# Optimization experiments

Hardware: AMD Instinct MI355X
Metric: run time of the kernel (lower is better)

The kernel has to match this reference:

```python
import jax, jax.numpy as jnp
import numpy as np

HEADS = 8
EPS = 1e-5
PW1 = (512, 8, 14, 14)   # (C, T, H, W), C = headsize1 * heads
PW2 = (512, 32, 7, 7)


def _ln(x, g, b):
    m = jnp.mean(x, axis=-1, keepdims=True)
    v = jnp.var(x, axis=-1, keepdims=True)
    return (x - m) * jax.lax.rsqrt(v + EPS) * g + b


def _mha(q, k, v):
    b, nq, c = q.shape
    nk = k.shape[1]
    hd = c // HEADS
    qh = q.reshape(b, nq, HEADS, hd).transpose(0, 2, 1, 3)  # [b,h,nq,hd]
    kh = k.reshape(b, nk, HEADS, hd).transpose(0, 2, 1, 3)
    vh = v.reshape(b, nk, HEADS, hd).transpose(0, 2, 1, 3)
    s = jnp.einsum('bhqd,bhkd->bhqk', qh, kh) * (hd ** -0.5)
    a = jax.nn.softmax(s, axis=-1)
    o = jnp.einsum('bhqk,bhkd->bhqd', a, vh)
    return o.transpose(0, 2, 1, 3).reshape(b, nq, c)


def _tok(x):
    b, c, t, h, w = x.shape
    return x.transpose(0, 2, 3, 4, 1).reshape(b, t * h * w, c)


def _detok(t, c, T, H, W):
    b = t.shape[0]
    return t.reshape(b, T, H, W, c).transpose(0, 4, 1, 2, 3)


def _out_head(y, w, bias, bn_g, bn_b):
    # 1x1x1 Conv3d + ReLU + BatchNorm3d (eval, running mean 0 / var 1)
    z = jnp.einsum('bcthw,oc->bothw', y, w) + bias[None, :, None, None, None]
    z = jax.nn.relu(z)
    z = z * jax.lax.rsqrt(jnp.float32(1.0 + EPS))
    return z * bn_g[None, :, None, None, None] + bn_b[None, :, None, None, None]


def reference(x1, x2, Wq1, bq1, Wk1, bk1, Wv1, bv1, ln1_g, ln1_b,
              Wq2, bq2, Wk2, bk2, Wv2, bv2, ln2_g, ln2_b,
              out1_w, out1_b, bn1_g, bn1_b, out2_w, out2_b, bn2_g, bn2_b):
    t1 = _tok(x1)  # [B, 1568, 512]
    t2 = _tok(x2)  # [B, 1568, 512]
    for i in range(3):  # three chained norm + cross-attn stages
        q1 = _ln(t1, ln1_g[i], ln1_b[i]) @ Wq1[i].T + bq1[i]
        k1 = t2 @ Wk1[i].T + bk1[i]
        v1 = t2 @ Wv1[i].T + bv1[i]
        q2 = _ln(t2, ln2_g[i], ln2_b[i]) @ Wq2[i].T + bq2[i]
        k2 = t1 @ Wk2[i].T + bk2[i]
        v2 = t1 @ Wv2[i].T + bv2[i]
        t1 = t1 + _mha(q1, k1, v1)
        t2 = t2 + _mha(q2, k2, v2)
    y1 = _detok(t1, *PW1)
    y2 = _detok(t2, *PW2)
    z1 = _out_head(y1, out1_w, out1_b, bn1_g, bn1_b)
    z2 = _out_head(y2, out2_w, out2_b, bn2_g, bn2_b)
    return (z1, z2)


def setup_inputs() -> dict:
    key = jax.random.key(0)
    ks = jax.random.split(key, 12)
    C = 512
    w = lambda k, shp: jax.random.normal(k, shp, jnp.float32) * 0.02
    return {
        'x1': jax.random.normal(ks[0], (4, C, 8, 14, 14), jnp.float32),
        'x2': jax.random.normal(ks[1], (4, C, 32, 7, 7), jnp.float32),
        'Wq1': w(ks[2], (3, C, C)), 'bq1': jnp.zeros((3, C), jnp.float32),
        'Wk1': w(ks[3], (3, C, C)), 'bk1': jnp.zeros((3, C), jnp.float32),
        'Wv1': w(ks[4], (3, C, C)), 'bv1': jnp.zeros((3, C), jnp.float32),
        'ln1_g': jnp.ones((3, C), jnp.float32), 'ln1_b': jnp.zeros((3, C), jnp.float32),
        'Wq2': w(ks[5], (3, C, C)), 'bq2': jnp.zeros((3, C), jnp.float32),
        'Wk2': w(ks[6], (3, C, C)), 'bk2': jnp.zeros((3, C), jnp.float32),
        'Wv2': w(ks[7], (3, C, C)), 'bv2': jnp.zeros((3, C), jnp.float32),
        'ln2_g': jnp.ones((3, C), jnp.float32), 'ln2_b': jnp.zeros((3, C), jnp.float32),
        'out1_w': w(ks[8], (C, C)), 'out1_b': jnp.zeros((C,), jnp.float32),
        'bn1_g': jnp.ones((C,), jnp.float32), 'bn1_b': jnp.zeros((C,), jnp.float32),
        'out2_w': w(ks[9], (C, C)), 'out2_b': jnp.zeros((C,), jnp.float32),
        'bn2_g': jnp.ones((C,), jnp.float32), 'bn2_b': jnp.zeros((C,), jnp.float32),
    }
```

## Files before the change

### kernel.cpp

```cpp
#include <hip/hip_runtime.h>

typedef __bf16 bf16_t;
typedef __bf16 bf16x8 __attribute__((ext_vector_type(8)));
typedef __bf16 bf16x4 __attribute__((ext_vector_type(4)));
typedef float f32x4 __attribute__((ext_vector_type(4)));
typedef float f32x16 __attribute__((ext_vector_type(16)));
typedef unsigned u32x4 __attribute__((ext_vector_type(4)));

#define NTOK 1568
#define CDIM 512
#define BATCH 4
#define MROWS (BATCH*NTOK)
#define RSQ1PEPS 0.9999950000374997f
#define CEXP 0.1803368801111204f
#define DEFER_THR 44.3614195558365f

__device__ __forceinline__ float fexp2(float x) {
  float r;
  asm("v_exp_f32 %0, %1" : "=v"(r) : "v"(x));
  return r;
}

__device__ __forceinline__ void glds16(const bf16_t* src, bf16_t* dst) {
  __builtin_amdgcn_global_load_lds(
      (const __attribute__((address_space(1))) unsigned*)src,
      (__attribute__((address_space(3))) unsigned*)dst, 16, 0, 0);
}

struct CastArgs { const float* s[20]; };
__global__ __launch_bounds__(256) void cast_kernel(CastArgs ca, bf16_t* __restrict__ out) {
  int idx = blockIdx.x * 256 + threadIdx.x;
  int m = idx >> 16;
  const float4* sp = (const float4*)ca.s[m];
  float4 v = sp[idx & 65535];
  bf16x4 o;
  o[0] = (bf16_t)v.x; o[1] = (bf16_t)v.y; o[2] = (bf16_t)v.z; o[3] = (bf16_t)v.w;
  *(bf16x4*)(out + (size_t)idx * 4) = o;
}

struct TokArgs { const float* x[2]; float* tf[2]; bf16_t* tb[2]; };
__global__ __launch_bounds__(256) void tok_kernel(TokArgs ta) {
  __shared__ float tile[32][33];
  int z = blockIdx.z, sel = z >> 2, b = z & 3;
  int c0 = blockIdx.y * 32, s0 = blockIdx.x * 32;
  int tx = threadIdx.x, ty = threadIdx.y;
  const float* xp = ta.x[sel] + (size_t)b * CDIM * NTOK;
  for (int r = 0; r < 32; r += 8)
    tile[ty + r][tx] = xp[(size_t)(c0 + ty + r) * NTOK + s0 + tx];
  __syncthreads();
  float* tfp = ta.tf[sel] + (size_t)b * NTOK * CDIM;
  bf16_t* tbp = ta.tb[sel] + (size_t)b * NTOK * CDIM;
  for (int r = 0; r < 32; r += 8) {
    float v = tile[tx][ty + r];
    size_t idx = (size_t)(s0 + ty + r) * CDIM + c0 + tx;
    tfp[idx] = v;
    tbp[idx] = (bf16_t)v;
  }
}

__global__ __launch_bounds__(64) void ln_kernel(
    const float* __restrict__ t1, const float* __restrict__ t2,
    const float* __restrict__ g1, const float* __restrict__ b1,
    const float* __restrict__ g2, const float* __restrict__ b2,
    bf16_t* __restrict__ o1, bf16_t* __restrict__ o2) {
  int row = blockIdx.x;
  const float* t; const float* g; const float* bt; bf16_t* out;
  if (row < MROWS) { t = t1; g = g1; bt = b1; out = o1; }
  else { row -= MROWS; t = t2; g = g2; bt = b2; out = o2; }
  int l = threadIdx.x;
  const float* x = t + (size_t)row * CDIM;
  float4 v0 = ((const float4*)x)[l];
  float4 v1 = ((const float4*)x)[l + 64];
  float s = v0.x + v0.y + v0.z + v0.w + v1.x + v1.y + v1.z + v1.w;
  float sq = v0.x*v0.x + v0.y*v0.y + v0.z*v0.z + v0.w*v0.w
           + v1.x*v1.x + v1.y*v1.y + v1.z*v1.z + v1.w*v1.w;
  for (int m = 1; m < 64; m <<= 1) { s += __shfl_xor(s, m); sq += __shfl_xor(sq, m); }
  float mean = s * (1.f / 512.f);
  float var = sq * (1.f / 512.f) - mean * mean;
  float rs = rsqrtf(var + 1e-5f);
  float4 g0 = ((const float4*)g)[l], g1v = ((const float4*)g)[l + 64];
  float4 b0 = ((const float4*)bt)[l], b1v = ((const float4*)bt)[l + 64];
  bf16x4 o0, o1v;
  o0[0] = (bf16_t)((v0.x - mean) * rs * g0.x + b0.x);
  o0[1] = (bf16_t)((v0.y - mean) * rs * g0.y + b0.y);
  o0[2] = (bf16_t)((v0.z - mean) * rs * g0.z + b0.z);
  o0[3] = (bf16_t)((v0.w - mean) * rs * g0.w + b0.w);
  o1v[0] = (bf16_t)((v1.x - mean) * rs * g1v.x + b1v.x);
  o1v[1] = (bf16_t)((v1.y - mean) * rs * g1v.y + b1v.y);
  o1v[2] = (bf16_t)((v1.z - mean) * rs * g1v.z + b1v.z);
  o1v[3] = (bf16_t)((v1.w - mean) * rs * g1v.w + b1v.w);
  *(bf16x4*)(out + (size_t)row * CDIM + l * 4) = o0;
  *(bf16x4*)(out + (size_t)row * CDIM + 256 + l * 4) = o1v;
}

template<int MODE>
__device__ __forceinline__ void gemm_core(
    bf16_t (* __restrict__ As)[40], bf16_t (* __restrict__ Bs)[40],
    const bf16_t* __restrict__ A, const bf16_t* __restrict__ Bp,
    const float* __restrict__ bias, const float* __restrict__ bng,
    const float* __restrict__ bnb, bf16_t* __restrict__ outb,
    float* __restrict__ outf, int m0, int n0, int Nvalid) {
  int tid = threadIdx.x;
  int w = tid >> 6, l = tid & 63, lr = l & 15, kg = l >> 4;
  int wm = (w >> 1) * 64, wn = (w & 1) * 64;
  f32x4 acc[4][4];
  for (int i = 0; i < 4; i++)
    for (int j = 0; j < 4; j++)
      acc[i][j] = f32x4{0.f, 0.f, 0.f, 0.f};
  int srow = tid >> 1;
  int soff = (tid & 1) * 16;
  int brow = n0 + srow;
  if (MODE != 0 && brow >= Nvalid) brow = Nvalid - 1;
  const bf16_t* aq = A + (size_t)(m0 + srow) * CDIM + soff;
  const bf16_t* bq = Bp + (size_t)brow * CDIM + soff;
  for (int kk = 0; kk < 16; kk++) {
    __syncthreads();
    bf16x8 a0 = *(const bf16x8*)(aq);
    bf16x8 a1 = *(const bf16x8*)(aq + 8);
    bf16x8 b0 = *(const bf16x8*)(bq);
    bf16x8 b1 = *(const bf16x8*)(bq + 8);
    aq += 32; bq += 32;
    *(bf16x8*)&As[srow][soff] = a0;
    *(bf16x8*)&As[srow][soff + 8] = a1;
    *(bf16x8*)&Bs[srow][soff] = b0;
    *(bf16x8*)&Bs[srow][soff + 8] = b1;
    __syncthreads();
    bf16x8 af[4], bfr[4];
    for (int i = 0; i < 4; i++) af[i] = *(const bf16x8*)&As[wm + i * 16 + lr][kg * 8];
    for (int j = 0; j < 4; j++) bfr[j] = *(const bf16x8*)&Bs[wn + j * 16 + lr][kg * 8];
    for (int i = 0; i < 4; i++)
      for (int j = 0; j < 4; j++)
        acc[i][j] = __builtin_amdgcn_mfma_f32_16x16x32_bf16(af[i], bfr[j], acc[i][j], 0, 0, 0);
  }
  for (int i = 0; i < 4; i++)
    for (int j = 0; j < 4; j++) {
      int rbase = m0 + wm + i * 16 + kg * 4;
      int col = n0 + wn + j * 16 + lr;
      for (int r = 0; r < 4; r++) {
        int row = rbase + r;
        float v = acc[i][j][r];
        if (MODE == 0) {
          v += bias[col];
          outb[(size_t)row * CDIM + col] = (bf16_t)v;
        } else if (MODE == 1) {
          v += bias[row];
          v = v > 0.f ? v : 0.f;
          v *= RSQ1PEPS;
          v = v * bng[row] + bnb[row];
          if (col < Nvalid) outf[(size_t)row * NTOK + col] = v;
        } else {
          v += bias[row];
          if (col < Nvalid) outb[(size_t)row * NTOK + col] = (bf16_t)v;
        }
      }
    }
}

struct ProjArgs {
  const bf16_t* A0[4]; const bf16_t* W0[4]; const float* b0[4]; bf16_t* o0[4];
  const bf16_t* W2[2]; const bf16_t* B2[2]; const float* b2[2]; bf16_t* o2[2];
};
__global__ __launch_bounds__(256) void proj_kernel(ProjArgs p) {
  __shared__ bf16_t As[128][40];
  __shared__ bf16_t Bs[128][40];
  int id = blockIdx.x;
  if (id < 784) {
    int set = id / 196, rem = id % 196;
    int n0 = (rem & 3) * 128, m0 = (rem >> 2) * 128;
    gemm_core<0>(As, Bs, p.A0[set], p.W0[set], p.b0[set], nullptr, nullptr,
                 p.o0[set], nullptr, m0, n0, 512);
  } else {
    int j = id - 784;
    int unit = j / 52;
    int which = unit >> 2, bat = unit & 3;
    int rem = j % 52;
    int n0 = (rem % 13) * 128, m0 = (rem / 13) * 128;
    gemm_core<2>(As, Bs, p.W2[which], p.B2[which] + (size_t)bat * NTOK * CDIM,
                 p.b2[which], nullptr, nullptr,
                 p.o2[which] + (size_t)bat * CDIM * NTOK, nullptr, m0, n0, NTOK);
  }
}

__global__ __launch_bounds__(256) void head_kernel(
    const bf16_t* __restrict__ W1, const bf16_t* __restrict__ W2,
    const bf16_t* __restrict__ t1b, const bf16_t* __restrict__ t2b,
    const float* __restrict__ b1, const float* __restrict__ b2,
    const float* __restrict__ bng1, const float* __restrict__ bnb1,
    const float* __restrict__ bng2, const float* __restrict__ bnb2,
    float* __restrict__ out) {
  __shared__ bf16_t As[128][40];
  __shared__ bf16_t Bs[128][40];
  int z = blockIdx.z;
  int which = z >> 2, bat = z & 3;
  const bf16_t* A = which ? W2 : W1;
  const bf16_t* Bp = (which ? t2b : t1b) + (size_t)bat * NTOK * CDIM;
  const float* bias = which ? b2 : b1;
  const float* bng = which ? bng2 : bng1;
  const float* bnb = which ? bnb2 : bnb1;
  float* outf = out + (size_t)which * BATCH * CDIM * NTOK + (size_t)bat * CDIM * NTOK;
  int m0 = blockIdx.y * 128, n0 = blockIdx.x * 128;
  gemm_core<1>(As, Bs, A, Bp, bias, bng, bnb, nullptr, outf, m0, n0, NTOK);
}

__device__ __forceinline__ float tree_max16(const f32x16& s) {
  float a0 = fmaxf(s[0], s[1]), a1 = fmaxf(s[2], s[3]);
  float a2 = fmaxf(s[4], s[5]), a3 = fmaxf(s[6], s[7]);
  float a4 = fmaxf(s[8], s[9]), a5 = fmaxf(s[10], s[11]);
  float a6 = fmaxf(s[12], s[13]), a7 = fmaxf(s[14], s[15]);
  a0 = fmaxf(a0, a1); a2 = fmaxf(a2, a3); a4 = fmaxf(a4, a5); a6 = fmaxf(a6, a7);
  return fmaxf(fmaxf(a0, a2), fmaxf(a4, a6));
}

__device__ __forceinline__ void build_frags(const float* p, bf16x8& Fa, bf16x8& Fb) {
  unsigned pk[8];
#pragma unroll
  for (int g = 0; g < 8; g++) {
    union { bf16_t hh[2]; unsigned u; } cv;
    cv.hh[0] = (bf16_t)p[2 * g];
    cv.hh[1] = (bf16_t)p[2 * g + 1];
    pk[g] = cv.u;
  }
  asm volatile("v_permlane32_swap_b32 %0, %1" : "+v"(pk[0]), "+v"(pk[2]));
  asm volatile("v_permlane32_swap_b32 %0, %1" : "+v"(pk[1]), "+v"(pk[3]));
  asm volatile("v_permlane32_swap_b32 %0, %1" : "+v"(pk[4]), "+v"(pk[6]));
  asm volatile("v_permlane32_swap_b32 %0, %1" : "+v"(pk[5]), "+v"(pk[7]));
  union { u32x4 u; bf16x8 bv; } A, B;
  A.u[0] = pk[0]; A.u[1] = pk[1]; A.u[2] = pk[2]; A.u[3] = pk[3];
  B.u[0] = pk[4]; B.u[1] = pk[5]; B.u[2] = pk[6]; B.u[3] = pk[7];
  Fa = A.bv; Fb = B.bv;
}

struct AttnArgs {
  const bf16_t* q[2]; const bf16_t* k[2]; const bf16_t* v[2];
  float* tf[2]; bf16_t* tb[2];
};

#define STAGE(TN, SL)                                                         \
  {                                                                           \
    int tnS_ = (TN); if (tnS_ > 48) tnS_ = 48;                                \
    glds16(kgl + (size_t)tnS_ * (32 * CDIM), &Ks[SL][wq8][0]);                \
    glds16(vgl + tnS_ * 32, &Vs[SL][wq16][0]);                                \
  }

#define QK(SL, SA)                                                            \
  {                                                                           \
    const bf16_t* kr_ = &Ks[SL][lo][0];                                       \
    __builtin_amdgcn_s_setprio(1);                                            \
    SA = __builtin_amdgcn_mfma_f32_32x32x16_bf16(                             \
        *(const bf16x8*)(kr_ + ((hi * 8) ^ sw3)), qf[0], z, 0, 0, 0);         \
    SA = __builtin_amdgcn_mfma_f32_32x32x16_bf16(                             \
        *(const bf16x8*)(kr_ + ((16 + hi * 8) ^ sw3)), qf[1], SA, 0, 0, 0);   \
    SA = __builtin_amdgcn_mfma_f32_32x32x16_bf16(                             \
        *(const bf16x8*)(kr_ + ((32 + hi * 8) ^ sw3)), qf[2], SA, 0, 0, 0);   \
    SA = __builtin_amdgcn_mfma_f32_32x32x16_bf16(                             \
        *(const bf16x8*)(kr_ + ((48 + hi * 8) ^ sw3)), qf[3], SA, 0, 0, 0);   \
    __builtin_amdgcn_s_setprio(0);                                            \
  }

#define FIN(SA, SL)                                                           \
  {                                                                           \
    float tm_ = tree_max16(SA);                                               \
    tm_ = fmaxf(tm_, __shfl_xor(tm_, 32));                                    \
    if (!__all(tm_ <= m_i + DEFER_THR)) {                                     \
      float mn_ = fmaxf(m_i, tm_);                                            \
      float al_ = fexp2((m_i - mn_) * CEXP);                                  \
      _Pragma("unroll")                                                       \
      for (int r_ = 0; r_ < 16; r_++) { ot0[r_] *= al_; ot1[r_] *= al_; }     \
      l_i *= al_;                                                             \
      m_i = mn_;                                                              \
    }                                                                         \
    float nmC_ = -m_i * CEXP;                                                 \
    float pa_[16];                                                            \
    _Pragma("unroll")                                                         \
    for (int r_ = 0; r_ < 16; r_++) pa_[r_] = fexp2(fmaf(SA[r_], CEXP, nmC_));\
    float ts_ = ((pa_[0]+pa_[1])+(pa_[2]+pa_[3]))+((pa_[4]+pa_[5])+(pa_[6]+pa_[7]))\
              + ((pa_[8]+pa_[9])+(pa_[10]+pa_[11]))+((pa_[12]+pa_[13])+(pa_[14]+pa_[15]));\
    ts_ += __shfl_xor(ts_, 32);                                               \
    l_i += ts_;                                                               \
    bf16x8 F0_, F1_;                                                          \
    build_frags(pa_, F0_, F1_);                                               \
    __builtin_amdgcn_s_setprio(1);                                            \
    ot0 = __builtin_amdgcn_mfma_f32_32x32x16_bf16(                            \
        *(const bf16x8*)(&Vs[SL][lo][(hi * 8) ^ sw2]), F0_, ot0, 0, 0, 0);    \
    ot0 = __builtin_amdgcn_mfma_f32_32x32x16_bf16(                            \
        *(const bf16x8*)(&Vs[SL][lo][(16 + hi * 8) ^ sw2]), F1_, ot0, 0, 0, 0);\
    ot1 = __builtin_amdgcn_mfma_f32_32x32x16_bf16(                            \
        *(const bf16x8*)(&Vs[SL][32 + lo][(hi * 8) ^ sw2]), F0_, ot1, 0, 0, 0);\
    ot1 = __builtin_amdgcn_mfma_f32_32x32x16_bf16(                            \
        *(const bf16x8*)(&Vs[SL][32 + lo][(16 + hi * 8) ^ sw2]), F1_, ot1, 0, 0, 0);\
    __builtin_amdgcn_s_setprio(0);                                            \
  }

#define STEP(T, SACUR, SAPRV, QSL, FSL, SSL)                                  \
  {                                                                           \
    STAGE((T) + 2, SSL);                                                      \
    QK(QSL, SACUR);                                                           \
    FIN(SAPRV, FSL);                                                          \
    asm volatile("s_waitcnt vmcnt(2)" ::: "memory");                          \
    __builtin_amdgcn_s_barrier();                                             \
  }

__global__ __launch_bounds__(256) void attn_kernel(AttnArgs aa) {
  __shared__ alignas(16) bf16_t Ks[4][32][64];
  __shared__ alignas(16) bf16_t Vs[4][64][32];
  int id = blockIdx.x;
  int xcd = id & 7, sl = id >> 3;
  int g = xcd + ((sl / 13) << 3);
  int qt = sl % 13;
  int ss = g >> 5, b = (g >> 3) & 3, h = g & 7;
  const bf16_t* qg = aa.q[ss];
  const bf16_t* kgp = aa.k[ss];
  const bf16_t* vtg = aa.v[ss];
  float* tf = aa.tf[ss];
  bf16_t* tb = aa.tb[ss];
  int tid = threadIdx.x, w = tid >> 6, l = tid & 63;
  int lo = l & 31, hi = l >> 5;
  int wq8 = w * 8, wq16 = w * 16;
  int sw3 = (lo & 7) << 3, sw2 = (lo & 3) << 3;
  const size_t kbase = ((size_t)b * NTOK) * CDIM + h * 64;
  const size_t vbase = ((size_t)b * CDIM + h * 64) * NTOK;

  int q0 = qt * 128 + w * 32;
  int qrow = q0 + lo;
  int qr = qrow < NTOK ? qrow : NTOK - 1;
  const bf16_t* qp = qg + kbase + (size_t)qr * CDIM + hi * 8;
  bf16x8 qf[4];
  qf[0] = *(const bf16x8*)(qp);
  qf[1] = *(const bf16x8*)(qp + 16);
  qf[2] = *(const bf16x8*)(qp + 32);
  qf[3] = *(const bf16x8*)(qp + 48);
  asm volatile("" : "+v"(qf[0]), "+v"(qf[1]), "+v"(qf[2]), "+v"(qf[3]));
  asm volatile("s_waitcnt vmcnt(0)" ::: "memory");

  const bf16_t* kgl = kgp + kbase + (size_t)(wq8 + (l >> 3)) * CDIM
                      + (((l & 7) ^ ((l >> 3) & 7)) << 3);
  const bf16_t* vgl = vtg + vbase + (size_t)(wq16 + (l >> 2)) * NTOK
                      + (((l & 3) ^ ((l >> 2) & 3)) << 3);

  float m_i = -3.0e38f, l_i = 0.f;
  f32x16 ot0, ot1, z, saA, saB;
#pragma unroll
  for (int r = 0; r < 16; r++) { ot0[r] = 0.f; ot1[r] = 0.f; z[r] = 0.f; }

  STAGE(0, 0);
  STAGE(1, 1);
  STAGE(2, 2);
  asm volatile("s_waitcnt vmcnt(2)" ::: "memory");
  __builtin_amdgcn_s_barrier();
  QK(0, saA);

  for (int t = 1; t <= 45; t += 4) {
    STEP(t + 0, saB, saA, 1, 0, 3);
    STEP(t + 1, saA, saB, 2, 1, 0);
    STEP(t + 2, saB, saA, 3, 2, 1);
    STEP(t + 3, saA, saB, 0, 3, 2);
  }
  FIN(saA, 0);

  if (qrow < NTOK) {
    float inv = 1.f / l_i;
    float* tfp = tf + ((size_t)b * NTOK + qrow) * CDIM + h * 64 + hi * 4;
    bf16_t* tbp = tb + ((size_t)b * NTOK + qrow) * CDIM + h * 64 + hi * 4;
#pragma unroll
    for (int db = 0; db < 2; db++) {
#pragma unroll
      for (int gq = 0; gq < 4; gq++) {
        int doff = db * 32 + gq * 8;
        float4 old = *(float4*)(tfp + doff);
        float4 nv;
        float a0 = (db ? ot1[gq * 4 + 0] : ot0[gq * 4 + 0]) * inv;
        float a1 = (db ? ot1[gq * 4 + 1] : ot0[gq * 4 + 1]) * inv;
        float a2 = (db ? ot1[gq * 4 + 2] : ot0[gq * 4 + 2]) * inv;
        float a3 = (db ? ot1[gq * 4 + 3] : ot0[gq * 4 + 3]) * inv;
        nv.x = old.x + a0; nv.y = old.y + a1; nv.z = old.z + a2; nv.w = old.w + a3;
        *(float4*)(tfp + doff) = nv;
        bf16x4 ob;
        ob[0] = (bf16_t)nv.x; ob[1] = (bf16_t)nv.y;
        ob[2] = (bf16_t)nv.z; ob[3] = (bf16_t)nv.w;
        *(bf16x4*)(tbp + doff) = ob;
      }
    }
  }
}

extern "C" void kernel_launch(void* const* d_in, const int* in_sizes, int n_in,
                              void* d_out, int out_size, void* d_ws, size_t ws_size,
                              hipStream_t stream) {
  (void)in_sizes; (void)n_in; (void)out_size; (void)ws_size;
  const float* x1 = (const float*)d_in[0];
  const float* x2 = (const float*)d_in[1];
  const float* Wq1 = (const float*)d_in[2];
  const float* bq1 = (const float*)d_in[3];
  const float* Wk1 = (const float*)d_in[4];
  const float* bk1 = (const float*)d_in[5];
  const float* Wv1 = (const float*)d_in[6];
  const float* bv1 = (const float*)d_in[7];
  const float* ln1_g = (const float*)d_in[8];
  const float* ln1_b = (const float*)d_in[9];
  const float* Wq2 = (const float*)d_in[10];
  const float* bq2 = (const float*)d_in[11];
  const float* Wk2 = (const float*)d_in[12];
  const float* bk2 = (const float*)d_in[13];
  const float* Wv2 = (const float*)d_in[14];
  const float* bv2 = (const float*)d_in[15];
  const float* ln2_g = (const float*)d_in[16];
  const float* ln2_b = (const float*)d_in[17];
  const float* out1_w = (const float*)d_in[18];
  const float* out1_b = (const float*)d_in[19];
  const float* bn1_g = (const float*)d_in[20];
  const float* bn1_b = (const float*)d_in[21];
  const float* out2_w = (const float*)d_in[22];
  const float* out2_b = (const float*)d_in[23];
  const float* bn2_g = (const float*)d_in[24];
  const float* bn2_b = (const float*)d_in[25];

  const size_t WMAT = 512 * 512;
  char* ws = (char*)d_ws;
  bf16_t* wb = (bf16_t*)ws;
  size_t off = 20 * WMAT * sizeof(bf16_t);
  float* t1f = (float*)(ws + off); off += (size_t)MROWS * CDIM * 4;
  float* t2f = (float*)(ws + off); off += (size_t)MROWS * CDIM * 4;
  bf16_t* t1b = (bf16_t*)(ws + off); off += (size_t)MROWS * CDIM * 2;
  bf16_t* t2b = (bf16_t*)(ws + off); off += (size_t)MROWS * CDIM * 2;
  bf16_t* l1b = (bf16_t*)(ws + off); off += (size_t)MROWS * CDIM * 2;
  bf16_t* l2b = (bf16_t*)(ws + off); off += (size_t)MROWS * CDIM * 2;
  bf16_t* q1b = (bf16_t*)(ws + off); off += (size_t)MROWS * CDIM * 2;
  bf16_t* k1b = (bf16_t*)(ws + off); off += (size_t)MROWS * CDIM * 2;
  bf16_t* v1b = (bf16_t*)(ws + off); off += (size_t)MROWS * CDIM * 2;
  bf16_t* q2b = (bf16_t*)(ws + off); off += (size_t)MROWS * CDIM * 2;
  bf16_t* k2b = (bf16_t*)(ws + off); off += (size_t)MROWS * CDIM * 2;
  bf16_t* v2b = (bf16_t*)(ws + off); off += (size_t)MROWS * CDIM * 2;

  CastArgs ca;
  for (int i = 0; i < 3; i++) {
    ca.s[0 + i] = Wq1 + (size_t)i * WMAT;
    ca.s[3 + i] = Wk1 + (size_t)i * WMAT;
    ca.s[6 + i] = Wv1 + (size_t)i * WMAT;
    ca.s[9 + i] = Wq2 + (size_t)i * WMAT;
    ca.s[12 + i] = Wk2 + (size_t)i * WMAT;
    ca.s[15 + i] = Wv2 + (size_t)i * WMAT;
  }
  ca.s[18] = out1_w;
  ca.s[19] = out2_w;
  cast_kernel<<<5120, 256, 0, stream>>>(ca, wb);

  TokArgs ta;
  ta.x[0] = x1; ta.x[1] = x2;
  ta.tf[0] = t1f; ta.tf[1] = t2f;
  ta.tb[0] = t1b; ta.tb[1] = t2b;
  tok_kernel<<<dim3(49, 16, 8), dim3(32, 8), 0, stream>>>(ta);

  AttnArgs aa;
  aa.q[0] = q1b; aa.q[1] = q2b;
  aa.k[0] = k1b; aa.k[1] = k2b;
  aa.v[0] = v1b; aa.v[1] = v2b;
  aa.tf[0] = t1f; aa.tf[1] = t2f;
  aa.tb[0] = t1b; aa.tb[1] = t2b;

  for (int i = 0; i < 3; i++) {
    ln_kernel<<<2 * MROWS, 64, 0, stream>>>(t1f, t2f,
        ln1_g + i * 512, ln1_b + i * 512, ln2_g + i * 512, ln2_b + i * 512,
        l1b, l2b);
    ProjArgs pa;
    pa.A0[0] = l1b; pa.W0[0] = wb + (0 + i) * WMAT; pa.b0[0] = bq1 + i * 512; pa.o0[0] = q1b;
    pa.A0[1] = t2b; pa.W0[1] = wb + (3 + i) * WMAT; pa.b0[1] = bk1 + i * 512; pa.o0[1] = k1b;
    pa.A0[2] = l2b; pa.W0[2] = wb + (9 + i) * WMAT; pa.b0[2] = bq2 + i * 512; pa.o0[2] = q2b;
    pa.A0[3] = t1b; pa.W0[3] = wb + (12 + i) * WMAT; pa.b0[3] = bk2 + i * 512; pa.o0[3] = k2b;
    pa.W2[0] = wb + (6 + i) * WMAT; pa.B2[0] = t2b; pa.b2[0] = bv1 + i * 512; pa.o2[0] = v1b;
    pa.W2[1] = wb + (15 + i) * WMAT; pa.B2[1] = t1b; pa.b2[1] = bv2 + i * 512; pa.o2[1] = v2b;
    proj_kernel<<<1200, 256, 0, stream>>>(pa);
    attn_kernel<<<832, 256, 0, stream>>>(aa);
  }

  float* out = (float*)d_out;
  head_kernel<<<dim3(13, 4, 8), 256, 0, stream>>>(
      wb + 18 * WMAT, wb + 19 * WMAT, t1b, t2b,
      out1_b, out2_b, bn1_g, bn1_b, bn2_g, bn2_b, out);
}
```

Baseline: 452.5 us.

## Split attention KV range in two and merge with LayerNorm-fused combine kernel

The attention kernel now splits each query tile's 49 key tiles into two halves processed by separate blocks (1664 instead of 832). It writes unnormalized bf16 partial outputs plus per-row max and sum to workspace. A new combine kernel merges the two partials with log-sum-exp weights, adds the residual, writes the fp32 and bf16 token copies, and computes the next stage's LayerNorm, which replaces the separate ln_kernel launch inside the loop. The aim is more parallelism on the 256-CU part and one fewer full pass over the tokens. The cost is a partial-output round trip through memory, an extra launch per stage, and bf16 rounding of the unnormalized partial outputs.

Measured after the change: 467.1 us. 3.2% more time.

```diff
diff --git a/kernel.cpp b/kernel.cpp
--- a/kernel.cpp
+++ b/kernel.cpp
@@ -14,6 +14,7 @@
 #define RSQ1PEPS 0.9999950000374997f
 #define CEXP 0.1803368801111204f
 #define DEFER_THR 44.3614195558365f
+#define PROWS 200704
 
 __device__ __forceinline__ float fexp2(float x) {
   float r;
@@ -232,14 +233,12 @@
 
 struct AttnArgs {
   const bf16_t* q[2]; const bf16_t* k[2]; const bf16_t* v[2];
-  float* tf[2]; bf16_t* tb[2];
 };
 
 #define STAGE(TN, SL)                                                         \
   {                                                                           \
-    int tnS_ = (TN); if (tnS_ > 48) tnS_ = 48;                                \
-    glds16(kgl + (size_t)tnS_ * (32 * CDIM), &Ks[SL][wq8][0]);                \
-    glds16(vgl + tnS_ * 32, &Vs[SL][wq16][0]);                                \
+    glds16(kgl + (size_t)(TN) * (32 * CDIM), &Ks[SL][wq8][0]);                \
+    glds16(vgl + (TN) * 32, &Vs[SL][wq16][0]);                                \
   }
 
 #define QK(SL, SA)                                                            \
@@ -291,28 +290,46 @@
     __builtin_amdgcn_s_setprio(0);                                            \
   }
 
-#define STEP(T, SACUR, SAPRV, QSL, FSL, SSL)                                  \
-  {                                                                           \
-    STAGE((T) + 2, SSL);                                                      \
-    QK(QSL, SACUR);                                                           \
-    FIN(SAPRV, FSL);                                                          \
-    asm volatile("s_waitcnt vmcnt(2)" ::: "memory");                          \
-    __builtin_amdgcn_s_barrier();                                             \
-  }
-
-__global__ __launch_bounds__(256) void attn_kernel(AttnArgs aa) {
+template<int NT>
+__device__ __forceinline__ void attn_core(
+    const bf16_t* kgl, const bf16_t* vgl,
+    bf16_t (*Ks)[32][64], bf16_t (*Vs)[64][32],
+    const bf16x8* qf, int lo, int hi, int sw3, int sw2, int wq8, int wq16,
+    float& m_i, float& l_i, f32x16& ot0, f32x16& ot1, const f32x16& z) {
+  f32x16 saA, saB;
+  STAGE(0, 0);
+  STAGE(1, 1);
+  STAGE(2, 2);
+  asm volatile("s_waitcnt vmcnt(2)" ::: "memory");
+  __builtin_amdgcn_s_barrier();
+  QK(0, saA);
+#pragma unroll
+  for (int t = 1; t < NT; ++t) {
+    int tn = (t + 2 > NT - 1) ? (NT - 1) : (t + 2);
+    STAGE(tn, (t + 2) & 3);
+    if (t & 1) { QK(t & 3, saB); FIN(saA, (t - 1) & 3); }
+    else       { QK(t & 3, saA); FIN(saB, (t - 1) & 3); }
+    asm volatile("s_waitcnt vmcnt(2)" ::: "memory");
+    __builtin_amdgcn_s_barrier();
+  }
+  if ((NT - 1) & 1) { FIN(saB, (NT - 1) & 3); }
+  else              { FIN(saA, (NT - 1) & 3); }
+}
+
+__global__ __launch_bounds__(256) void attn_kernel(
+    AttnArgs aa, bf16_t* __restrict__ po, float* __restrict__ pm,
+    float* __restrict__ pl) {
   __shared__ alignas(16) bf16_t Ks[4][32][64];
   __shared__ alignas(16) bf16_t Vs[4][64][32];
   int id = blockIdx.x;
   int xcd = id & 7, sl = id >> 3;
-  int g = xcd + ((sl / 13) << 3);
-  int qt = sl % 13;
+  int g = xcd + ((sl / 26) << 3);
+  int rem = sl % 26;
+  int qt = rem >> 1, sp = rem & 1;
   int ss = g >> 5, b = (g >> 3) & 3, h = g & 7;
   const bf16_t* qg = aa.q[ss];
   const bf16_t* kgp = aa.k[ss];
   const bf16_t* vtg = aa.v[ss];
-  float* tf = aa.tf[ss];
-  bf16_t* tb = aa.tb[ss];
   int tid = threadIdx.x, w = tid >> 6, l = tid & 63;
   int lo = l & 31, hi = l >> 5;
   int wq8 = w * 8, wq16 = w * 16;
@@ -338,48 +355,108 @@
                       + (((l & 3) ^ ((l >> 2) & 3)) << 3);
 
   float m_i = -3.0e38f, l_i = 0.f;
-  f32x16 ot0, ot1, z, saA, saB;
+  f32x16 ot0, ot1, z;
 #pragma unroll
   for (int r = 0; r < 16; r++) { ot0[r] = 0.f; ot1[r] = 0.f; z[r] = 0.f; }
 
-  STAGE(0, 0);
-  STAGE(1, 1);
-  STAGE(2, 2);
-  asm volatile("s_waitcnt vmcnt(2)" ::: "memory");
-  __builtin_amdgcn_s_barrier();
-  QK(0, saA);
-
-  for (int t = 1; t <= 45; t += 4) {
-    STEP(t + 0, saB, saA, 1, 0, 3);
-    STEP(t + 1, saA, saB, 2, 1, 0);
-    STEP(t + 2, saB, saA, 3, 2, 1);
-    STEP(t + 3, saA, saB, 0, 3, 2);
-  }
-  FIN(saA, 0);
+  if (sp == 0) {
+    attn_core<25>(kgl, vgl, Ks, Vs, qf, lo, hi, sw3, sw2, wq8, wq16,
+                  m_i, l_i, ot0, ot1, z);
+  } else {
+    attn_core<24>(kgl + (size_t)25 * 32 * CDIM, vgl + 25 * 32, Ks, Vs,
+                  qf, lo, hi, sw3, sw2, wq8, wq16,
+                  m_i, l_i, ot0, ot1, z);
+  }
 
   if (qrow < NTOK) {
-    float inv = 1.f / l_i;
-    float* tfp = tf + ((size_t)b * NTOK + qrow) * CDIM + h * 64 + hi * 4;
-    bf16_t* tbp = tb + ((size_t)b * NTOK + qrow) * CDIM + h * 64 + hi * 4;
+    size_t prow = ((((size_t)ss * 4 + b) * 8 + h) * 2 + sp) * NTOK + qrow;
+    bf16_t* pop = po + prow * 64 + hi * 4;
 #pragma unroll
     for (int db = 0; db < 2; db++) {
 #pragma unroll
       for (int gq = 0; gq < 4; gq++) {
         int doff = db * 32 + gq * 8;
-        float4 old = *(float4*)(tfp + doff);
-        float4 nv;
-        float a0 = (db ? ot1[gq * 4 + 0] : ot0[gq * 4 + 0]) * inv;
-        float a1 = (db ? ot1[gq * 4 + 1] : ot0[gq * 4 + 1]) * inv;
-        float a2 = (db ? ot1[gq * 4 + 2] : ot0[gq * 4 + 2]) * inv;
-        float a3 = (db ? ot1[gq * 4 + 3] : ot0[gq * 4 + 3]) * inv;
-        nv.x = old.x + a0; nv.y = old.y + a1; nv.z = old.z + a2; nv.w = old.w + a3;
-        *(float4*)(tfp + doff) = nv;
         bf16x4 ob;
-        ob[0] = (bf16_t)nv.x; ob[1] = (bf16_t)nv.y;
-        ob[2] = (bf16_t)nv.z; ob[3] = (bf16_t)nv.w;
-        *(bf16x4*)(tbp + doff) = ob;
+        ob[0] = (bf16_t)(db ? ot1[gq * 4 + 0] : ot0[gq * 4 + 0]);
+        ob[1] = (bf16_t)(db ? ot1[gq * 4 + 1] : ot0[gq * 4 + 1]);
+        ob[2] = (bf16_t)(db ? ot1[gq * 4 + 2] : ot0[gq * 4 + 2]);
+        ob[3] = (bf16_t)(db ? ot1[gq * 4 + 3] : ot0[gq * 4 + 3]);
+        *(bf16x4*)(pop + doff) = ob;
       }
     }
+    if (hi == 0) { pm[prow] = m_i; pl[prow] = l_i; }
+  }
+}
+
+template<bool DOLN>
+__global__ __launch_bounds__(256) void combine_kernel(
+    const bf16_t* __restrict__ po, const float* __restrict__ pm,
+    const float* __restrict__ pl,
+    float* __restrict__ t1f, float* __restrict__ t2f,
+    bf16_t* __restrict__ t1b, bf16_t* __restrict__ t2b,
+    const float* __restrict__ g1, const float* __restrict__ bt1,
+    const float* __restrict__ g2, const float* __restrict__ bt2,
+    bf16_t* __restrict__ l1b, bf16_t* __restrict__ l2b) {
+  int tid = threadIdx.x;
+  int r = blockIdx.x * 4 + (tid >> 6);
+  int l = tid & 63;
+  int s = r / (BATCH * NTOK);
+  int rem = r - s * (BATCH * NTOK);
+  int b = rem / NTOK;
+  int q = rem - b * NTOK;
+  int h = l >> 3, d0 = (l & 7) * 8;
+  size_t p0 = ((((size_t)s * 4 + b) * 8 + h) * 2) * NTOK + q;
+  size_t p1 = p0 + NTOK;
+  float m0 = pm[p0], m1 = pm[p1];
+  float l0 = pl[p0], l1v = pl[p1];
+  float mx = fmaxf(m0, m1);
+  float w0 = fexp2((m0 - mx) * CEXP);
+  float w1 = fexp2((m1 - mx) * CEXP);
+  float linv = 1.f / (l0 * w0 + l1v * w1);
+  w0 *= linv; w1 *= linv;
+  bf16x8 a = *(const bf16x8*)(po + p0 * 64 + d0);
+  bf16x8 c = *(const bf16x8*)(po + p1 * 64 + d0);
+  size_t tbase = ((size_t)b * NTOK + q) * CDIM + l * 8;
+  float* tf = (s ? t2f : t1f) + tbase;
+  bf16_t* tb = (s ? t2b : t1b) + tbase;
+  float4 o0 = ((float4*)tf)[0], o1 = ((float4*)tf)[1];
+  float nv[8];
+  nv[0] = o0.x + ((float)a[0] * w0 + (float)c[0] * w1);
+  nv[1] = o0.y + ((float)a[1] * w0 + (float)c[1] * w1);
+  nv[2] = o0.z + ((float)a[2] * w0 + (float)c[2] * w1);
+  nv[3] = o0.w + ((float)a[3] * w0 + (float)c[3] * w1);
+  nv[4] = o1.x + ((float)a[4] * w0 + (float)c[4] * w1);
+  nv[5] = o1.y + ((float)a[5] * w0 + (float)c[5] * w1);
+  nv[6] = o1.z + ((float)a[6] * w0 + (float)c[6] * w1);
+  nv[7] = o1.w + ((float)a[7] * w0 + (float)c[7] * w1);
+  ((float4*)tf)[0] = float4{nv[0], nv[1], nv[2], nv[3]};
+  ((float4*)tf)[1] = float4{nv[4], nv[5], nv[6], nv[7]};
+  bf16x8 ob;
+#pragma unroll
+  for (int j = 0; j < 8; j++) ob[j] = (bf16_t)nv[j];
+  *(bf16x8*)tb = ob;
+  if (DOLN) {
+    float sum = 0.f, sq = 0.f;
+#pragma unroll
+    for (int j = 0; j < 8; j++) { sum += nv[j]; sq += nv[j] * nv[j]; }
+    for (int m = 1; m < 64; m <<= 1) { sum += __shfl_xor(sum, m); sq += __shfl_xor(sq, m); }
+    float mean = sum * (1.f / 512.f);
+    float var = sq * (1.f / 512.f) - mean * mean;
+    float rs = rsqrtf(var + 1e-5f);
+    const float* g = s ? g2 : g1;
+    const float* bt = s ? bt2 : bt1;
+    float4 gv0 = ((const float4*)(g + l * 8))[0], gv1 = ((const float4*)(g + l * 8))[1];
+    float4 bv0 = ((const float4*)(bt + l * 8))[0], bv1 = ((const float4*)(bt + l * 8))[1];
+    bf16x8 lb;
+    lb[0] = (bf16_t)((nv[0] - mean) * rs * gv0.x + bv0.x);
+    lb[1] = (bf16_t)((nv[1] - mean) * rs * gv0.y + bv0.y);
+    lb[2] = (bf16_t)((nv[2] - mean) * rs * gv0.z + bv0.z);
+    lb[3] = (bf16_t)((nv[3] - mean) * rs * gv0.w + bv0.w);
+    lb[4] = (bf16_t)((nv[4] - mean) * rs * gv1.x + bv1.x);
+    lb[5] = (bf16_t)((nv[5] - mean) * rs * gv1.y + bv1.y);
+    lb[6] = (bf16_t)((nv[6] - mean) * rs * gv1.z + bv1.z);
+    lb[7] = (bf16_t)((nv[7] - mean) * rs * gv1.w + bv1.w);
+    *(bf16x8*)((s ? l2b : l1b) + tbase) = lb;
   }
 }
 
@@ -430,6 +507,9 @@
   bf16_t* q2b = (bf16_t*)(ws + off); off += (size_t)MROWS * CDIM * 2;
   bf16_t* k2b = (bf16_t*)(ws + off); off += (size_t)MROWS * CDIM * 2;
   bf16_t* v2b = (bf16_t*)(ws + off); off += (size_t)MROWS * CDIM * 2;
+  bf16_t* po = (bf16_t*)(ws + off); off += (size_t)PROWS * 64 * 2;
+  float* pm = (float*)(ws + off); off += (size_t)PROWS * 4;
+  float* pl = (float*)(ws + off); off += (size_t)PROWS * 4;
 
   CastArgs ca;
   for (int i = 0; i < 3; i++) {
@@ -450,17 +530,15 @@
   ta.tb[0] = t1b; ta.tb[1] = t2b;
   tok_kernel<<<dim3(49, 16, 8), dim3(32, 8), 0, stream>>>(ta);
 
+  ln_kernel<<<2 * MROWS, 64, 0, stream>>>(t1f, t2f,
+      ln1_g, ln1_b, ln2_g, ln2_b, l1b, l2b);
+
   AttnArgs aa;
   aa.q[0] = q1b; aa.q[1] = q2b;
   aa.k[0] = k1b; aa.k[1] = k2b;
   aa.v[0] = v1b; aa.v[1] = v2b;
-  aa.tf[0] = t1f; aa.tf[1] = t2f;
-  aa.tb[0] = t1b; aa.tb[1] = t2b;
 
   for (int i = 0; i < 3; i++) {
-    ln_kernel<<<2 * MROWS, 64, 0, stream>>>(t1f, t2f,
-        ln1_g + i * 512, ln1_b + i * 512, ln2_g + i * 512, ln2_b + i * 512,
-        l1b, l2b);
     ProjArgs pa;
     pa.A0[0] = l1b; pa.W0[0] = wb + (0 + i) * WMAT; pa.b0[0] = bq1 + i * 512; pa.o0[0] = q1b;
     pa.A0[1] = t2b; pa.W0[1] = wb + (3 + i) * WMAT; pa.b0[1] = bk1 + i * 512; pa.o0[1] = k1b;
@@ -469,7 +547,15 @@
     pa.W2[0] = wb + (6 + i) * WMAT; pa.B2[0] = t2b; pa.b2[0] = bv1 + i * 512; pa.o2[0] = v1b;
     pa.W2[1] = wb + (15 + i) * WMAT; pa.B2[1] = t1b; pa.b2[1] = bv2 + i * 512; pa.o2[1] = v2b;
     proj_kernel<<<1200, 256, 0, stream>>>(pa);
-    attn_kernel<<<832, 256, 0, stream>>>(aa);
+    attn_kernel<<<1664, 256, 0, stream>>>(aa, po, pm, pl);
+    if (i < 2) {
+      combine_kernel<true><<<3136, 256, 0, stream>>>(po, pm, pl, t1f, t2f, t1b, t2b,
+          ln1_g + (i + 1) * 512, ln1_b + (i + 1) * 512,
+          ln2_g + (i + 1) * 512, ln2_b + (i + 1) * 512, l1b, l2b);
+    } else {
+      combine_kernel<false><<<3136, 256, 0, stream>>>(po, pm, pl, t1f, t2f, t1b, t2b,
+          nullptr, nullptr, nullptr, nullptr, nullptr, nullptr);
+    }
   }
 
   float* out = (float*)d_out;
```
